# Kernel tuning notes

Measured on AMD Instinct MI355X. Metric: run time of the kernel, lower is better.

## Reference

```python
import jax, jax.numpy as jnp
import numpy as np
import math

NUM_CLASS = 100000
EMB = 512
N = 1024
S = 64.0
M2 = 0.5
M3 = 0.2
T = 0.2
ERRSUM = 0.3
CLEAR_RIO = 1.0 - ERRSUM
NUM_ALL = 2900.0
GAMMA = 2
EMA = 0.01


def setup_inputs() -> dict:
    key = jax.random.key(0)
    k1, k2, k3 = jax.random.split(key, 3)
    logits = jax.random.normal(k1, (N, EMB), dtype=jnp.float32)
    labels = jax.random.randint(k2, (N,), 0, NUM_CLASS, dtype=jnp.int64)
    weight = jax.random.normal(k3, (NUM_CLASS, EMB), dtype=jnp.float32) * 0.01
    return {"logits": logits, "labels": labels, "weight": weight}


def _l2norm(x):
    return x * jax.lax.rsqrt(jnp.sum(x * x, axis=-1, keepdims=True) + 1e-12)


def reference(logits, labels, weight):
    # margin constants (m_smooth starts at 0, so margin_ada leaves m3 unchanged)
    cos_m, sin_m = math.cos(M2), math.sin(M2)
    theta = math.cos(math.pi - M2)
    sinmm = math.sin(math.pi - M2) * M2
    cos_m_, sin_m_ = math.cos(M3), math.sin(M3)
    sinmm_ = math.sin(-M3) * M3

    # cosine similarity GEMM: [N, C]
    cos = jnp.clip(_l2norm(logits) @ _l2norm(weight).T, -1.0, 1.0)

    rows = jnp.arange(cos.shape[0])
    tgt = cos[rows, labels]                       # [N]
    sin_theta = jnp.sqrt(1.0 - tgt * tgt)
    cos_theta_m = tgt * cos_m - sin_theta * sin_m
    cos_theta_m_ = tgt * cos_m_ - sin_theta * sin_m_
    ftl = jnp.where(tgt > theta, cos_theta_m, tgt - sinmm)          # hard margin
    ftl_ = jnp.where(tgt <= cos_m_, cos_theta_m_, tgt + sinmm_)     # noise margin

    mask_hard = cos > ftl[:, None]
    mask_noise = cos > ftl_[:, None]

    # m_smooth update (pure counting -> non-differentiable constant)
    hard_cnt = jnp.sum(mask_hard).astype(jnp.float32)
    m_smooth = ((NUM_ALL - hard_cnt) / NUM_ALL) * EMA  # prev m_smooth = 0
    noise_scale = (1.0 - m_smooth / CLEAR_RIO) ** GAMMA

    out = jnp.where(mask_hard, cos * (T + 1.0), cos)
    out = jnp.where(mask_noise, jnp.maximum(cos * noise_scale, 1e-30), out)
    out = out.at[rows, labels].set(ftl)
    return out * S
```

## Files before the change

kernel.cpp:

```cpp
#include <hip/hip_runtime.h>
#include <hip/hip_bf16.h>
#include <stdint.h>

#define NUM_CLASS 100000
#define CPAD      100096
#define EMB       512
#define NROW      1024

#define BM 128
#define BN 128
#define BK 64

typedef __bf16 bf16x8 __attribute__((ext_vector_type(8)));
typedef float  f32x4  __attribute__((ext_vector_type(4)));

#define WS_FTL  256
#define WS_FTL2 4352
#define WS_A    8704
#define WS_B    1057280

__device__ inline unsigned short f2bf(float x) {
    uint32_t u = __builtin_bit_cast(uint32_t, x);
    uint32_t r = u + 0x7FFFu + ((u >> 16) & 1u);
    return (unsigned short)(r >> 16);
}
__device__ inline unsigned int pack2(float a, float b) {
    return (unsigned int)f2bf(a) | ((unsigned int)f2bf(b) << 16);
}

__device__ __forceinline__ void gld16(const unsigned short* g, unsigned short* l) {
    __builtin_amdgcn_global_load_lds(
        (const __attribute__((address_space(1))) unsigned int*)g,
        (__attribute__((address_space(3))) unsigned int*)l,
        16, 0, 0);
}

__global__ __launch_bounds__(256) void prep_a(const float* __restrict__ logits,
                                              unsigned short* __restrict__ A) {
    int wave = threadIdx.x >> 6, lane = threadIdx.x & 63;
    int row = blockIdx.x * 4 + wave;
    const float4* src = (const float4*)(logits + (size_t)row * EMB + lane * 8);
    float4 a = src[0], b = src[1];
    float ss = a.x*a.x + a.y*a.y + a.z*a.z + a.w*a.w
             + b.x*b.x + b.y*b.y + b.z*b.z + b.w*b.w;
    for (int off = 32; off; off >>= 1) ss += __shfl_xor(ss, off, 64);
    float rs = rsqrtf(ss + 1e-12f);
    uint4 o;
    o.x = pack2(a.x*rs, a.y*rs); o.y = pack2(a.z*rs, a.w*rs);
    o.z = pack2(b.x*rs, b.y*rs); o.w = pack2(b.z*rs, b.w*rs);
    *(uint4*)(A + (size_t)row * EMB + lane * 8) = o;
}

__global__ __launch_bounds__(256) void prep_b(const float* __restrict__ w,
                                              unsigned short* __restrict__ B) {
    int wave = threadIdx.x >> 6, lane = threadIdx.x & 63;
    int row = blockIdx.x * 4 + wave;
    uint4 o = {0u, 0u, 0u, 0u};
    if (row < NUM_CLASS) {
        const float4* src = (const float4*)(w + (size_t)row * EMB + lane * 8);
        float4 a = src[0], b = src[1];
        float ss = a.x*a.x + a.y*a.y + a.z*a.z + a.w*a.w
                 + b.x*b.x + b.y*b.y + b.z*b.z + b.w*b.w;
        for (int off = 32; off; off >>= 1) ss += __shfl_xor(ss, off, 64);
        float rs = rsqrtf(ss + 1e-12f);
        o.x = pack2(a.x*rs, a.y*rs); o.y = pack2(a.z*rs, a.w*rs);
        o.z = pack2(b.x*rs, b.y*rs); o.w = pack2(b.z*rs, b.w*rs);
    }
    *(uint4*)(B + (size_t)row * EMB + lane * 8) = o;
}

__global__ __launch_bounds__(64) void prep_rows(const float* __restrict__ logits,
                                                const float* __restrict__ w,
                                                const int* __restrict__ labels,
                                                float* __restrict__ ftl,
                                                float* __restrict__ ftl2,
                                                unsigned int* __restrict__ cnt) {
    int row = blockIdx.x, lane = threadIdx.x;
    if (row == 0 && lane == 0) *cnt = 0u;
    int lab = labels[row];
    const float4* lp = (const float4*)(logits + (size_t)row * EMB + lane * 8);
    const float4* wp = (const float4*)(w + (size_t)lab * EMB + lane * 8);
    float4 l0 = lp[0], l1 = lp[1], w0 = wp[0], w1 = wp[1];
    float sl = l0.x*l0.x + l0.y*l0.y + l0.z*l0.z + l0.w*l0.w
             + l1.x*l1.x + l1.y*l1.y + l1.z*l1.z + l1.w*l1.w;
    float sw = w0.x*w0.x + w0.y*w0.y + w0.z*w0.z + w0.w*w0.w
             + w1.x*w1.x + w1.y*w1.y + w1.z*w1.z + w1.w*w1.w;
    float d  = l0.x*w0.x + l0.y*w0.y + l0.z*w0.z + l0.w*w0.w
             + l1.x*w1.x + l1.y*w1.y + l1.z*w1.z + l1.w*w1.w;
    for (int off = 32; off; off >>= 1) {
        sl += __shfl_xor(sl, off, 64);
        sw += __shfl_xor(sw, off, 64);
        d  += __shfl_xor(d,  off, 64);
    }
    if (lane == 0) {
        float tgt = d * rsqrtf(sl + 1e-12f) * rsqrtf(sw + 1e-12f);
        tgt = fminf(1.0f, fmaxf(-1.0f, tgt));
        const float cos_m  = 0.8775825618903728f;
        const float sin_m  = 0.479425538604203f;
        const float theta  = -0.8775825618903728f;
        const float sinmm  = 0.2397127693021015f;
        const float cos_m_ = 0.9800665778412416f;
        const float sin_m_ = 0.19866933079506122f;
        const float sinmm_ = -0.03973386615901225f;
        float st   = sqrtf(fmaxf(0.0f, 1.0f - tgt * tgt));
        float ctm  = tgt * cos_m  - st * sin_m;
        float ctm_ = tgt * cos_m_ - st * sin_m_;
        ftl[row]  = (tgt > theta)    ? ctm  : (tgt - sinmm);
        ftl2[row] = (tgt <= cos_m_)  ? ctm_ : (tgt + sinmm_);
    }
}

__global__ __launch_bounds__(256) void gemm_count(const unsigned short* __restrict__ A,
                                                  const unsigned short* __restrict__ B,
                                                  const float* __restrict__ ftl,
                                                  float* __restrict__ out,
                                                  unsigned int* __restrict__ cnt) {
    __shared__ __align__(16) unsigned short lA[BM * BK];
    __shared__ __align__(16) unsigned short lB[BN * BK];
    int tid = threadIdx.x;
    int wave = tid >> 6, lane = tid & 63;
    int wm = wave >> 1, wn = wave & 1;
    int quad = lane >> 4, l16 = lane & 15;
    int bm = blockIdx.x, bn = blockIdx.y;

    f32x4 acc[4][4] = {};

    int srow  = tid >> 3;
    int sslot = tid & 7;
    const unsigned short* a_src = A + ((size_t)bm * BM + srow) * EMB + sslot * 8;
    const unsigned short* b_src = B + ((size_t)bn * BN + srow) * EMB + sslot * 8;
    unsigned short* a_dst = &lA[tid * 8];
    unsigned short* b_dst = &lB[tid * 8];

#pragma unroll 1
    for (int kk = 0; kk < EMB / BK; ++kk) {
        int k0 = kk * BK;
#pragma unroll
        for (int r = 0; r < 4; ++r) {
            gld16(a_src + (size_t)r * 32 * EMB + k0, a_dst + r * 32 * BK);
            gld16(b_src + (size_t)r * 32 * EMB + k0, b_dst + r * 32 * BK);
        }
        __syncthreads();
#pragma unroll
        for (int ks = 0; ks < 2; ++ks) {
            bf16x8 af[4], bfr[4];
#pragma unroll
            for (int i = 0; i < 4; ++i) {
                int ar = wm * 64 + i * 16 + l16;
                af[i]  = *(const bf16x8*)&lA[ar * BK + ks * 32 + quad * 8];
                int br = wn * 64 + i * 16 + l16;
                bfr[i] = *(const bf16x8*)&lB[br * BK + ks * 32 + quad * 8];
            }
#pragma unroll
            for (int i = 0; i < 4; ++i)
#pragma unroll
                for (int j = 0; j < 4; ++j)
                    acc[i][j] = __builtin_amdgcn_mfma_f32_16x16x32_bf16(af[i], bfr[j], acc[i][j], 0, 0, 0);
        }
        __syncthreads();
    }

    int local = 0;
#pragma unroll
    for (int i = 0; i < 4; ++i) {
        int row0 = bm * BM + wm * 64 + i * 16 + quad * 4;
        float f0 = ftl[row0], f1 = ftl[row0 + 1], f2 = ftl[row0 + 2], f3 = ftl[row0 + 3];
#pragma unroll
        for (int j = 0; j < 4; ++j) {
            int col = bn * BN + wn * 64 + j * 16 + l16;
            bool cv = col < NUM_CLASS;
#pragma unroll
            for (int r = 0; r < 4; ++r) {
                float c = acc[i][j][r];
                c = fminf(1.0f, fmaxf(-1.0f, c));
                if (cv) {
                    float fr = (r == 0) ? f0 : (r == 1) ? f1 : (r == 2) ? f2 : f3;
                    local += (c > fr) ? 1 : 0;
                    out[(size_t)(row0 + r) * NUM_CLASS + col] = c;
                }
            }
        }
    }
    for (int off = 32; off; off >>= 1) local += __shfl_down(local, off, 64);
    if (lane == 0) atomicAdd(cnt, (unsigned int)local);
}

__global__ __launch_bounds__(256) void apply_k(float* __restrict__ out,
                                               const float* __restrict__ ftl,
                                               const float* __restrict__ ftl2,
                                               const int* __restrict__ labels,
                                               const unsigned int* __restrict__ cnt) {
    int idx = blockIdx.x * 256 + threadIdx.x;
    int row = idx / 25000;
    int c4  = idx - row * 25000;
    float h = (float)(*cnt);
    float msm = ((2900.0f - h) / 2900.0f) * 0.01f;
    float t = 1.0f - msm / 0.7f;
    float ns = t * t;
    float f = ftl[row], f2 = ftl2[row];
    int lab = labels[row];
    float4* p = (float4*)(out + (size_t)row * NUM_CLASS) + c4;
    float4 v = *p;
    float r[4] = {v.x, v.y, v.z, v.w};
    int col = c4 * 4;
#pragma unroll
    for (int q = 0; q < 4; ++q) {
        float c = r[q];
        float o = (c > f) ? c * 1.2f : c;
        if (c > f2) o = fmaxf(c * ns, 1e-30f);
        if (col + q == lab) o = f;
        r[q] = o * 64.0f;
    }
    *p = make_float4(r[0], r[1], r[2], r[3]);
}

extern "C" void kernel_launch(void* const* d_in, const int* in_sizes, int n_in,
                              void* d_out, int out_size, void* d_ws, size_t ws_size,
                              hipStream_t stream) {
    const float* logits = (const float*)d_in[0];
    const int*   labels = (const int*)d_in[1];
    const float* weight = (const float*)d_in[2];
    char* ws = (char*)d_ws;
    unsigned int*  cnt  = (unsigned int*)ws;
    float*         ftl  = (float*)(ws + WS_FTL);
    float*         ftl2 = (float*)(ws + WS_FTL2);
    unsigned short* A   = (unsigned short*)(ws + WS_A);
    unsigned short* B   = (unsigned short*)(ws + WS_B);
    float* out = (float*)d_out;

    prep_a<<<NROW / 4, 256, 0, stream>>>(logits, A);
    prep_b<<<CPAD / 4, 256, 0, stream>>>(weight, B);
    prep_rows<<<NROW, 64, 0, stream>>>(logits, weight, labels, ftl, ftl2, cnt);
    gemm_count<<<dim3(NROW / BM, CPAD / BN), 256, 0, stream>>>(A, B, ftl, out, cnt);
    apply_k<<<100000, 256, 0, stream>>>(out, ftl, ftl2, labels, cnt);
}
```

Before: 982.8 us.

## Widen GEMM tile, swizzle LDS, remap blocks per XCD, loop apply kernel

Widens the GEMM N tile from 128 to 256, so each wave computes 4x8 MFMA tiles and reuses its A fragments across more B columns. Applies an XOR swizzle to the LDS layout to cut bank conflicts. Remaps the 1D block index so the blocks sharing a B tile land on the same XCD for L2 reuse. Changes the apply kernel to 4096 blocks that each stride over a quarter row, in place of 100000 one-shot blocks, which avoids the per-element divide. The trade-off is more accumulator registers and more LDS per block, which may lower occupancy. It also pads the B tile loads up to CPAD.

```diff
diff --git a/kernel.cpp b/kernel.cpp
--- a/kernel.cpp
+++ b/kernel.cpp
@@ -8,8 +8,10 @@
 #define NROW      1024
 
 #define BM 128
-#define BN 128
+#define BN 256
 #define BK 64
+#define NBN 391
+#define NBM 8
 
 typedef __bf16 bf16x8 __attribute__((ext_vector_type(8)));
 typedef float  f32x4  __attribute__((ext_vector_type(4)));
@@ -121,14 +123,20 @@
     int wave = tid >> 6, lane = tid & 63;
     int wm = wave >> 1, wn = wave & 1;
     int quad = lane >> 4, l16 = lane & 15;
-    int bm = blockIdx.x, bn = blockIdx.y;
-
-    f32x4 acc[4][4] = {};
+    int sw = l16 & 7;
+
+    int f  = blockIdx.x;
+    int wg = (f & 7) * NBN + (f >> 3);
+    int bm = wg & 7;
+    int bn = wg >> 3;
+
+    f32x4 acc[4][8] = {};
 
     int srow  = tid >> 3;
     int sslot = tid & 7;
-    const unsigned short* a_src = A + ((size_t)bm * BM + srow) * EMB + sslot * 8;
-    const unsigned short* b_src = B + ((size_t)bn * BN + srow) * EMB + sslot * 8;
+    int sg    = sslot ^ (srow & 7);
+    const unsigned short* a_src = A + ((size_t)(bm * BM + srow)) * EMB + sg * 8;
+    const unsigned short* b_src = B + ((size_t)(bn * BN + srow)) * EMB + sg * 8;
     unsigned short* a_dst = &lA[tid * 8];
     unsigned short* b_dst = &lB[tid * 8];
 
@@ -136,25 +144,29 @@
     for (int kk = 0; kk < EMB / BK; ++kk) {
         int k0 = kk * BK;
 #pragma unroll
-        for (int r = 0; r < 4; ++r) {
-            gld16(a_src + (size_t)r * 32 * EMB + k0, a_dst + r * 32 * BK);
-            gld16(b_src + (size_t)r * 32 * EMB + k0, b_dst + r * 32 * BK);
-        }
+        for (int r = 0; r < 4; ++r)
+            gld16(a_src + (size_t)r * 32 * EMB + k0, a_dst + r * 2048);
+#pragma unroll
+        for (int r = 0; r < 8; ++r)
+            gld16(b_src + (size_t)r * 32 * EMB + k0, b_dst + r * 2048);
         __syncthreads();
 #pragma unroll
         for (int ks = 0; ks < 2; ++ks) {
-            bf16x8 af[4], bfr[4];
+            bf16x8 af[4], bfr[8];
 #pragma unroll
             for (int i = 0; i < 4; ++i) {
                 int ar = wm * 64 + i * 16 + l16;
-                af[i]  = *(const bf16x8*)&lA[ar * BK + ks * 32 + quad * 8];
-                int br = wn * 64 + i * 16 + l16;
-                bfr[i] = *(const bf16x8*)&lB[br * BK + ks * 32 + quad * 8];
+                af[i]  = *(const bf16x8*)&lA[ar * BK + (((ks * 4 + quad) ^ sw) << 3)];
             }
 #pragma unroll
+            for (int j = 0; j < 8; ++j) {
+                int br = wn * 128 + j * 16 + l16;
+                bfr[j] = *(const bf16x8*)&lB[br * BK + (((ks * 4 + quad) ^ sw) << 3)];
+            }
+#pragma unroll
             for (int i = 0; i < 4; ++i)
 #pragma unroll
-                for (int j = 0; j < 4; ++j)
+                for (int j = 0; j < 8; ++j)
                     acc[i][j] = __builtin_amdgcn_mfma_f32_16x16x32_bf16(af[i], bfr[j], acc[i][j], 0, 0, 0);
         }
         __syncthreads();
@@ -166,8 +178,8 @@
         int row0 = bm * BM + wm * 64 + i * 16 + quad * 4;
         float f0 = ftl[row0], f1 = ftl[row0 + 1], f2 = ftl[row0 + 2], f3 = ftl[row0 + 3];
 #pragma unroll
-        for (int j = 0; j < 4; ++j) {
-            int col = bn * BN + wn * 64 + j * 16 + l16;
+        for (int j = 0; j < 8; ++j) {
+            int col = bn * BN + wn * 128 + j * 16 + l16;
             bool cv = col < NUM_CLASS;
 #pragma unroll
             for (int r = 0; r < 4; ++r) {
@@ -190,28 +202,30 @@
                                                const float* __restrict__ ftl2,
                                                const int* __restrict__ labels,
                                                const unsigned int* __restrict__ cnt) {
-    int idx = blockIdx.x * 256 + threadIdx.x;
-    int row = idx / 25000;
-    int c4  = idx - row * 25000;
-    float h = (float)(*cnt);
+    int row     = blockIdx.x >> 2;
+    int quarter = blockIdx.x & 3;
+    float h   = (float)(*cnt);
     float msm = ((2900.0f - h) / 2900.0f) * 0.01f;
-    float t = 1.0f - msm / 0.7f;
-    float ns = t * t;
-    float f = ftl[row], f2 = ftl2[row];
-    int lab = labels[row];
-    float4* p = (float4*)(out + (size_t)row * NUM_CLASS) + c4;
-    float4 v = *p;
-    float r[4] = {v.x, v.y, v.z, v.w};
-    int col = c4 * 4;
-#pragma unroll
-    for (int q = 0; q < 4; ++q) {
-        float c = r[q];
-        float o = (c > f) ? c * 1.2f : c;
-        if (c > f2) o = fmaxf(c * ns, 1e-30f);
-        if (col + q == lab) o = f;
-        r[q] = o * 64.0f;
-    }
-    *p = make_float4(r[0], r[1], r[2], r[3]);
+    float t   = 1.0f - msm / 0.7f;
+    float ns  = t * t;
+    float fv  = ftl[row], f2v = ftl2[row];
+    int   lab = labels[row];
+    float4* base = (float4*)(out + (size_t)row * NUM_CLASS);
+    int c4end = (quarter + 1) * 6250;
+    for (int c4 = quarter * 6250 + (int)threadIdx.x; c4 < c4end; c4 += 256) {
+        float4 v = base[c4];
+        float r[4] = {v.x, v.y, v.z, v.w};
+        int col = c4 * 4;
+#pragma unroll
+        for (int q = 0; q < 4; ++q) {
+            float c = r[q];
+            float o = (c > fv) ? c * 1.2f : c;
+            if (c > f2v) o = fmaxf(c * ns, 1e-30f);
+            if (col + q == lab) o = fv;
+            r[q] = o * 64.0f;
+        }
+        base[c4] = make_float4(r[0], r[1], r[2], r[3]);
+    }
 }
 
 extern "C" void kernel_launch(void* const* d_in, const int* in_sizes, int n_in,
@@ -231,6 +245,6 @@
     prep_a<<<NROW / 4, 256, 0, stream>>>(logits, A);
     prep_b<<<CPAD / 4, 256, 0, stream>>>(weight, B);
     prep_rows<<<NROW, 64, 0, stream>>>(logits, weight, labels, ftl, ftl2, cnt);
-    gemm_count<<<dim3(NROW / BM, CPAD / BN), 256, 0, stream>>>(A, B, ftl, out, cnt);
-    apply_k<<<100000, 256, 0, stream>>>(out, ftl, ftl2, labels, cnt);
-}
+    gemm_count<<<NBM * NBN, 256, 0, stream>>>(A, B, ftl, out, cnt);
+    apply_k<<<4096, 256, 0, stream>>>(out, ftl, ftl2, labels, cnt);
+}
```

Result: slower. 1.101 ms (+12.0%).
